# Optimization experiments

Hardware: AMD Instinct MI355X
Metric: run time of the kernel (lower is better)

Reference implementation:

```python
import jax, jax.numpy as jnp
import numpy as np

# Module constants (match init_kwargs / input_specs)
B, Q, K, DM, H, F, S = 2, 2048, 2048, 512, 8, 5, 2
DH = DM // H  # head dim = 64


def setup_inputs() -> dict:
    key = jax.random.key(0)
    ks_ = jax.random.split(key, 18)
    sc = 1.0 / np.sqrt(DM)
    inp = {
        'qs': jax.random.normal(ks_[0], (B, Q, DM), jnp.float32),
        'ks': jax.random.normal(ks_[1], (B, K, DM), jnp.float32),
        'vs': jax.random.normal(ks_[2], (B, K, DM), jnp.float32),
        'qs_locs': jax.random.uniform(ks_[3], (B, Q, S), jnp.float32) * 10.0,
        'ks_locs': jax.random.uniform(ks_[4], (B, K, S), jnp.float32) * 10.0,
        # projection weights (MLP([512]) == single Dense(512))
        'Wq': jax.random.normal(ks_[5], (DM, DM), jnp.float32) * sc,
        'bq': jnp.zeros((DM,), jnp.float32),
        'Wk': jax.random.normal(ks_[6], (DM, DM), jnp.float32) * sc,
        'bk': jnp.zeros((DM,), jnp.float32),
        'Wv': jax.random.normal(ks_[7], (DM, DM), jnp.float32) * sc,
        'bv': jnp.zeros((DM,), jnp.float32),
        'Wo': jax.random.normal(ks_[8], (DM, DM), jnp.float32) * sc,
        'bo': jnp.zeros((DM,), jnp.float32),
        # TISA RBF params, one triple per (head, basis); init near module defaults (1,1,0)
        'a': 1.0 + 0.1 * jax.random.normal(ks_[9], (H * F,), jnp.float32),
        'b': 1.0 + 0.1 * jax.random.normal(ks_[10], (H * F,), jnp.float32),
        'c': 0.1 * jax.random.normal(ks_[11], (H * F,), jnp.float32),
        # valid lens in [K//2, K] so every row has at least one valid key
        'valid_lens': jax.random.randint(ks_[12], (B,), K // 2, K + 1).astype(jnp.int32),
    }
    return inp


def reference(qs, ks, vs, qs_locs, ks_locs, Wq, bq, Wk, bk, Wv, bv, Wo, bo, a, b, c, valid_lens):
    # Projections and head split
    q = (qs @ Wq + bq).reshape(B, Q, H, DH) / jnp.sqrt(jnp.float32(DH))
    k = (ks @ Wk + bk).reshape(B, K, H, DH)
    v = (vs @ Wv + bv).reshape(B, K, H, DH)

    # Pairwise L2 distance between query and key locations: [B, Q, K]
    diff = qs_locs[:, :, None, :] - ks_locs[:, None, :, :]
    d = jnp.sqrt(jnp.sum(diff * diff, axis=-1))

    # TISA RBF bias, summed over F basis functions per head: [B, H, Q, K]
    aH, bH, cH = a.reshape(H, F), b.reshape(H, F), c.reshape(H, F)
    bias = jnp.zeros((B, H, Q, K), jnp.float32)
    for f in range(F):  # small fixed loop over basis functions
        af = aH[:, f][None, :, None, None]
        bf = jnp.abs(bH[:, f])[None, :, None, None]
        cf = cH[:, f][None, :, None, None]
        bias = bias + af * jnp.exp(-bf * (d[:, None] - cf) ** 2)

    scores = jnp.einsum('bqhd,bkhd->bhqk', q, k) + bias
    mask = (jnp.arange(K)[None, :] < valid_lens[:, None])[:, None, None, :]  # [B,1,1,K]
    scores = jnp.where(mask, scores, -jnp.inf)
    p = jax.nn.softmax(scores, axis=-1)  # identical to the online-softmax scan result
    ctx = jnp.einsum('bhqk,bkhd->bqhd', p, v).reshape(B, Q, DM)
    return ctx @ Wo + bo
```

## Files before the change

### kernel.cpp

```cpp
#include <hip/hip_runtime.h>
#include <hip/hip_fp16.h>

typedef unsigned short u16;
typedef __bf16 bf16x8 __attribute__((ext_vector_type(8)));
typedef float f32x4 __attribute__((ext_vector_type(4)));
typedef float f32x16 __attribute__((ext_vector_type(16)));

#define MFMA16(a, b, c) __builtin_amdgcn_mfma_f32_16x16x32_bf16(a, b, c, 0, 0, 0)
#define MFMA32(a, b, c) __builtin_amdgcn_mfma_f32_32x32x16_bf16(a, b, c, 0, 0, 0)

constexpr float LOG2E = 1.44269504088896340736f;

__device__ __forceinline__ u16 f2bf(float x) {
  unsigned u = __float_as_uint(x);
  u += 0x7fffu + ((u >> 16) & 1u);
  return (u16)(u >> 16);
}
__device__ __forceinline__ u16 f2bf_fast(float x) {
  return (u16)((__float_as_uint(x) + 0x8000u) >> 16);
}

struct FalseT { static constexpr bool value = false; };
struct TrueT  { static constexpr bool value = true;  };

__global__ void transpose_w_kernel(const float* __restrict__ w0, const float* __restrict__ w1,
                                   const float* __restrict__ w2, const float* __restrict__ w3,
                                   u16* __restrict__ wt) {
  __shared__ float tile[32][33];
  const float* W = blockIdx.z == 0 ? w0 : blockIdx.z == 1 ? w1 : blockIdx.z == 2 ? w2 : w3;
  u16* T = wt + (size_t)blockIdx.z * 512 * 512;
  int tx = threadIdx.x, ty = threadIdx.y;
  int x = blockIdx.x * 32 + tx;
  int y0 = blockIdx.y * 32;
#pragma unroll
  for (int i = 0; i < 32; i += 8) tile[ty + i][tx] = W[(y0 + ty + i) * 512 + x];
  __syncthreads();
  int xo = blockIdx.y * 32 + tx;
  int r0 = blockIdx.x * 32;
#pragma unroll
  for (int i = 0; i < 32; i += 8) T[(r0 + ty + i) * 512 + xo] = f2bf(tile[tx][ty + i]);
}

__global__ __launch_bounds__(256) void qkv_gemm(
    const float* __restrict__ qs, const float* __restrict__ ks, const float* __restrict__ vs,
    const u16* __restrict__ Wt, const float* __restrict__ bq, const float* __restrict__ bk,
    const float* __restrict__ bv, u16* __restrict__ qg, u16* __restrict__ kg,
    u16* __restrict__ vTg) {
  __shared__ u16 As[128 * 72];
  __shared__ u16 Bs[64 * 72];
  const int tid = threadIdx.x;
  const int wave = tid >> 6, lane = tid & 63;
  const int l15 = lane & 15, quad = lane >> 4;
  const int id = blockIdx.x;
  const bool qk = id < 512;
  int z = 0, m0, n0;
  const float* Af = nullptr;
  const u16* Ab = nullptr;
  const u16* Bb = nullptr;
  const float* Bf = nullptr;
  if (qk) {
    z = id >> 8;
    int t = id & 255;
    m0 = (t >> 3) * 128;
    n0 = (t & 7) * 64;
    Af = z ? ks : qs;
    Bb = Wt + z * 262144;
  } else {
    int t = id - 512;
    m0 = (t >> 6) * 128;
    n0 = (t & 63) * 64;
    Ab = Wt + 2 * 262144;
    Bf = vs;
  }
  f32x4 acc[2][4];
#pragma unroll
  for (int i = 0; i < 2; i++)
#pragma unroll
    for (int j = 0; j < 4; j++) {
      f32x4 zr = {0.f, 0.f, 0.f, 0.f};
      acc[i][j] = zr;
    }
  const int srA = tid >> 1, scA = (tid & 1) * 32;
  const int srB = tid >> 2, scB = (tid & 3) * 16;
  for (int k0 = 0; k0 < 512; k0 += 64) {
    if (qk) {
      const float* ga = Af + (m0 + srA) * 512 + k0 + scA;
      u16* la = As + srA * 72 + scA;
#pragma unroll
      for (int c = 0; c < 4; ++c) {
        float4 f0 = *(const float4*)(ga + c * 8);
        float4 f1 = *(const float4*)(ga + c * 8 + 4);
        uint4 u;
        u.x = f2bf(f0.x) | ((unsigned)f2bf(f0.y) << 16);
        u.y = f2bf(f0.z) | ((unsigned)f2bf(f0.w) << 16);
        u.z = f2bf(f1.x) | ((unsigned)f2bf(f1.y) << 16);
        u.w = f2bf(f1.z) | ((unsigned)f2bf(f1.w) << 16);
        *(uint4*)(la + c * 8) = u;
      }
      const u16* gb = Bb + (n0 + srB) * 512 + k0 + scB;
      u16* lb = Bs + srB * 72 + scB;
      *(uint4*)(lb) = *(const uint4*)(gb);
      *(uint4*)(lb + 8) = *(const uint4*)(gb + 8);
    } else {
      const u16* ga = Ab + (m0 + srA) * 512 + k0 + scA;
      u16* la = As + srA * 72 + scA;
#pragma unroll
      for (int c = 0; c < 4; ++c) *(uint4*)(la + c * 8) = *(const uint4*)(ga + c * 8);
      const float* gb = Bf + (n0 + srB) * 512 + k0 + scB;
      u16* lb = Bs + srB * 72 + scB;
#pragma unroll
      for (int c = 0; c < 2; ++c) {
        float4 f0 = *(const float4*)(gb + c * 8);
        float4 f1 = *(const float4*)(gb + c * 8 + 4);
        uint4 u;
        u.x = f2bf(f0.x) | ((unsigned)f2bf(f0.y) << 16);
        u.y = f2bf(f0.z) | ((unsigned)f2bf(f0.w) << 16);
        u.z = f2bf(f1.x) | ((unsigned)f2bf(f1.y) << 16);
        u.w = f2bf(f1.z) | ((unsigned)f2bf(f1.w) << 16);
        *(uint4*)(lb + c * 8) = u;
      }
    }
    __syncthreads();
#pragma unroll
    for (int st = 0; st < 2; ++st) {
      bf16x8 af[2], bfr[4];
#pragma unroll
      for (int mt = 0; mt < 2; ++mt)
        af[mt] = *(const bf16x8*)(As + (wave * 32 + mt * 16 + l15) * 72 + st * 32 + quad * 8);
#pragma unroll
      for (int nt = 0; nt < 4; ++nt)
        bfr[nt] = *(const bf16x8*)(Bs + (nt * 16 + l15) * 72 + st * 32 + quad * 8);
#pragma unroll
      for (int mt = 0; mt < 2; ++mt)
#pragma unroll
        for (int nt = 0; nt < 4; ++nt) acc[mt][nt] = MFMA16(af[mt], bfr[nt], acc[mt][nt]);
    }
    __syncthreads();
  }
  if (qk) {
    const float* bias = z ? bk : bq;
    const float scale = z ? 1.0f : 0.125f * LOG2E;
#pragma unroll
    for (int mt = 0; mt < 2; ++mt)
#pragma unroll
      for (int nt = 0; nt < 4; ++nt)
#pragma unroll
        for (int r = 0; r < 4; ++r) {
          int row = m0 + wave * 32 + mt * 16 + quad * 4 + r;
          int col = n0 + nt * 16 + l15;
          float v = (acc[mt][nt][r] + bias[col]) * scale;
          int b = row >> 11, key = row & 2047, hh = col >> 6, dh = col & 63;
          int bhh = b * 8 + hh;
          if (z == 0) {
            qg[((bhh * 2048) + key) * 64 + dh] = f2bf(v);
          } else {
            int kt = key >> 6, tt = (key >> 5) & 1, lk = key & 31;
            int st = dh >> 4, hif = (dh >> 3) & 1, j = dh & 7;
            kg[(size_t)(bhh * 32 + kt) * 4096 + tt * 2048 + st * 512 + (hif * 32 + lk) * 8 +
               j] = f2bf(v);
          }
        }
  } else {
#pragma unroll
    for (int mt = 0; mt < 2; ++mt)
#pragma unroll
      for (int nt = 0; nt < 4; ++nt)
#pragma unroll
        for (int r = 0; r < 4; ++r) {
          int row = m0 + wave * 32 + mt * 16 + quad * 4 + r;
          int col = n0 + nt * 16 + l15;
          int hh = row >> 6, dh = row & 63, b = col >> 11, key = col & 2047;
          int bhh = b * 8 + hh;
          int kt = key >> 6, kk = key & 63, st = kk >> 4, hif = (kk >> 3) & 1, j = kk & 7;
          int h2 = dh >> 5, lk = dh & 31;
          vTg[(size_t)(bhh * 32 + kt) * 4096 + h2 * 2048 + st * 512 + (hif * 32 + lk) * 8 + j] =
              f2bf(acc[mt][nt][r] + bv[row]);
        }
  }
}

__global__ __launch_bounds__(256, 4) void attn_kernel(
    const u16* __restrict__ qg, const u16* __restrict__ kfrag, const u16* __restrict__ vfrag,
    const float* __restrict__ qlocs, const float* __restrict__ klocs,
    const float* __restrict__ aP, const float* __restrict__ bP, const float* __restrict__ cP,
    const int* __restrict__ vlen, u16* __restrict__ Opart, float* __restrict__ lpart) {
  constexpr int TBLN = 2048;
  constexpr float DMAX = 14.16f;
  constexpr float TSCALE = (float)TBLN / DMAX;
  __shared__ u16 Ps[4][32 * 68];
  __shared__ alignas(16) float2 klb[576];
  __shared__ float tbl[TBLN];
  const int tid = threadIdx.x;
  const int wave = tid >> 6, lane = tid & 63;
  const int l31 = lane & 31, hi = lane >> 5;
  const int bh = blockIdx.y, b = bh >> 3, h = bh & 7;
  const int z = blockIdx.z;
  const int vl = vlen[b];
  const int ntiles = (vl + 63) >> 6;
  const int nfull = vl >> 6;
  const int tb = ntiles >> 2, rem = ntiles & 3;
  const int kt0 = z * tb + (z < rem ? z : rem);
  const int ktend = kt0 + tb + (z < rem ? 1 : 0);

  for (int i = tid; i < TBLN; i += 256) {
    float d = (i + 0.5f) * (DMAX / TBLN);
    float g = 0.f;
#pragma unroll
    for (int f = 0; f < 5; ++f) {
      float t = d - cP[h * 5 + f];
      g += aP[h * 5 + f] * __expf(-fabsf(bP[h * 5 + f]) * t * t);
    }
    tbl[i] = g * LOG2E;
  }
  const int nk = (ktend - kt0) * 64;
  for (int i = tid; i < nk; i += 256) {
    float2 kl = *(const float2*)(klocs + (b * 2048 + kt0 * 64 + i) * 2);
    klb[i] = make_float2(kl.x * TSCALE, kl.y * TSCALE);
  }
  __syncthreads();

  const int qrow = blockIdx.x * 128 + wave * 32 + l31;
  bf16x8 aq[4];
  {
    const u16* qr = qg + (bh * 2048 + qrow) * 64 + hi * 8;
#pragma unroll
    for (int st = 0; st < 4; ++st) aq[st] = *(const bf16x8*)(qr + st * 16);
  }
  float qpx, qpy;
  {
    float2 p = *(const float2*)(qlocs + (b * 2048 + qrow) * 2);
    qpx = p.x * TSCALE;
    qpy = p.y * TSCALE;
  }
  float l_ = 0.f;
  f32x16 oacc[2];
#pragma unroll
  for (int i = 0; i < 2; ++i)
#pragma unroll
    for (int j = 0; j < 16; ++j) oacc[i][j] = 0.f;
  u16* pw = Ps[wave];

  auto tile = [&](int kt, auto mc) {
    constexpr bool MASKED = decltype(mc)::value;
    const int k0 = kt * 64;
    const int rt64 = (kt - kt0) * 64;
    const u16* fb = kfrag + (size_t)(bh * 32 + kt) * 4096 + lane * 8;
    const u16* vb = vfrag + (size_t)(bh * 32 + kt) * 4096 + lane * 8;
#pragma unroll
    for (int t = 0; t < 2; ++t) {
      bf16x8 kf[4];
#pragma unroll
      for (int st = 0; st < 4; ++st)
        kf[st] = *(const bf16x8*)(fb + t * 2048 + st * 512);
      f32x16 s;
#pragma unroll
      for (int j = 0; j < 16; ++j) s[j] = 0.f;
#pragma unroll
      for (int st = 0; st < 4; ++st) s = MFMA32(kf[st], aq[st], s);
#pragma unroll
      for (int g = 0; g < 4; ++g) {
        const int kl0 = t * 32 + hi * 4 + g * 8;
        float4 ka = *(const float4*)(&klb[rt64 + kl0]);
        float4 kb = *(const float4*)(&klb[rt64 + kl0 + 2]);
        float kx[4] = {ka.x, ka.z, kb.x, kb.z};
        float ky[4] = {ka.y, ka.w, kb.y, kb.w};
        float p[4];
#pragma unroll
        for (int j = 0; j < 4; ++j) {
          float dx = qpx - kx[j], dy = qpy - ky[j];
          float t_ = __builtin_amdgcn_sqrtf(fmaf(dx, dx, dy * dy));
          int ti = (int)t_;
          float v = s[g * 4 + j] + tbl[ti];
          if (MASKED) v = (k0 + kl0 + j < vl) ? v : -1e30f;
          p[j] = __builtin_amdgcn_exp2f(v);
          l_ += p[j];
        }
        uint2 w;
        w.x = f2bf_fast(p[0]) | ((unsigned)f2bf_fast(p[1]) << 16);
        w.y = f2bf_fast(p[2]) | ((unsigned)f2bf_fast(p[3]) << 16);
        *(uint2*)(pw + l31 * 68 + kl0) = w;
      }
    }
    __asm__ volatile("s_waitcnt lgkmcnt(0)" ::: "memory");
    bf16x8 vf[2][4];
#pragma unroll
    for (int h2 = 0; h2 < 2; ++h2)
#pragma unroll
      for (int st = 0; st < 4; ++st)
        vf[h2][st] = *(const bf16x8*)(vb + h2 * 2048 + st * 512);
#pragma unroll
    for (int st = 0; st < 4; ++st) {
      bf16x8 pf = *(const bf16x8*)(pw + l31 * 68 + st * 16 + hi * 8);
#pragma unroll
      for (int h2 = 0; h2 < 2; ++h2) oacc[h2] = MFMA32(vf[h2][st], pf, oacc[h2]);
    }
  };

  const int fullend = ktend < nfull ? ktend : nfull;
  for (int kt = kt0; kt < fullend; ++kt) tile(kt, FalseT{});
  if (ktend > nfull) tile(nfull, TrueT{});

  l_ += __shfl_xor(l_, 32);
  if (hi == 0) lpart[z * 32768 + bh * 2048 + qrow] = l_;
  u16* ob = Opart + ((size_t)(z * 16 + bh) * 2048 + qrow) * 64;
#pragma unroll
  for (int h2 = 0; h2 < 2; ++h2)
#pragma unroll
    for (int g = 0; g < 4; ++g) {
      const int dh0 = h2 * 32 + hi * 4 + g * 8;
      uint2 w;
      w.x = f2bf(oacc[h2][g * 4 + 0]) | ((unsigned)f2bf(oacc[h2][g * 4 + 1]) << 16);
      w.y = f2bf(oacc[h2][g * 4 + 2]) | ((unsigned)f2bf(oacc[h2][g * 4 + 3]) << 16);
      *(uint2*)(ob + dh0) = w;
    }
}

__global__ __launch_bounds__(256) void combine_kernel(const u16* __restrict__ Opart,
                                                      const float* __restrict__ lpart,
                                                      u16* __restrict__ ctxb) {
  const int t = blockIdx.x * 256 + threadIdx.x;
  const int dh8 = (t & 7) * 8;
  const int row = t >> 3;
  float l = 0.f;
#pragma unroll
  for (int zz = 0; zz < 4; ++zz) l += lpart[zz * 32768 + row];
  const float inv = 1.f / l;
  float vals[8];
#pragma unroll
  for (int j = 0; j < 8; ++j) vals[j] = 0.f;
#pragma unroll
  for (int zz = 0; zz < 4; ++zz) {
    bf16x8 o8 = *(const bf16x8*)(Opart + ((size_t)(zz * 32768) + row) * 64 + dh8);
#pragma unroll
    for (int j = 0; j < 8; ++j) vals[j] += (float)o8[j];
  }
  const int bh = row >> 11, q = row & 2047;
  const int b = bh >> 3, h = bh & 7;
  uint4 u;
  u.x = f2bf(vals[0] * inv) | ((unsigned)f2bf(vals[1] * inv) << 16);
  u.y = f2bf(vals[2] * inv) | ((unsigned)f2bf(vals[3] * inv) << 16);
  u.z = f2bf(vals[4] * inv) | ((unsigned)f2bf(vals[5] * inv) << 16);
  u.w = f2bf(vals[6] * inv) | ((unsigned)f2bf(vals[7] * inv) << 16);
  *(uint4*)(ctxb + ((size_t)(b * 2048 + q) * 512 + h * 64 + dh8)) = u;
}

__global__ __launch_bounds__(256) void out_gemm(const u16* __restrict__ ctxb,
                                                const u16* __restrict__ Wt,
                                                const float* __restrict__ bo,
                                                float* __restrict__ out) {
  __shared__ u16 As[64 * 72];
  __shared__ u16 Bs[64 * 72];
  const u16* WoT = Wt + 3 * 262144;
  const int tid = threadIdx.x;
  const int wave = tid >> 6, lane = tid & 63;
  const int l15 = lane & 15, quad = lane >> 4;
  const int m0 = blockIdx.x * 64, n0 = blockIdx.y * 64;
  f32x4 acc[4];
#pragma unroll
  for (int j = 0; j < 4; j++) {
    f32x4 zr = {0.f, 0.f, 0.f, 0.f};
    acc[j] = zr;
  }
  const int sr = tid >> 2, sc = (tid & 3) * 16;
  for (int k0 = 0; k0 < 512; k0 += 64) {
    const u16* ga = ctxb + (m0 + sr) * 512 + k0 + sc;
    u16* la = As + sr * 72 + sc;
    *(uint4*)(la) = *(const uint4*)(ga);
    *(uint4*)(la + 8) = *(const uint4*)(ga + 8);
    const u16* gb = WoT + (n0 + sr) * 512 + k0 + sc;
    u16* lb = Bs + sr * 72 + sc;
    *(uint4*)(lb) = *(const uint4*)(gb);
    *(uint4*)(lb + 8) = *(const uint4*)(gb + 8);
    __syncthreads();
#pragma unroll
    for (int st = 0; st < 2; ++st) {
      bf16x8 af = *(const bf16x8*)(As + (wave * 16 + l15) * 72 + st * 32 + quad * 8);
#pragma unroll
      for (int nt = 0; nt < 4; ++nt) {
        bf16x8 bfr = *(const bf16x8*)(Bs + (nt * 16 + l15) * 72 + st * 32 + quad * 8);
        acc[nt] = MFMA16(af, bfr, acc[nt]);
      }
    }
    __syncthreads();
  }
#pragma unroll
  for (int nt = 0; nt < 4; ++nt)
#pragma unroll
    for (int r = 0; r < 4; ++r) {
      int rrow = m0 + wave * 16 + quad * 4 + r;
      int col = n0 + nt * 16 + l15;
      out[rrow * 512 + col] = acc[nt][r] + bo[col];
    }
}

extern "C" void kernel_launch(void* const* d_in, const int* in_sizes, int n_in, void* d_out,
                              int out_size, void* d_ws, size_t ws_size, hipStream_t stream) {
  const float* qs = (const float*)d_in[0];
  const float* ks = (const float*)d_in[1];
  const float* vs = (const float*)d_in[2];
  const float* qlocs = (const float*)d_in[3];
  const float* klocs = (const float*)d_in[4];
  const float* Wq = (const float*)d_in[5];
  const float* bq = (const float*)d_in[6];
  const float* Wk = (const float*)d_in[7];
  const float* bk = (const float*)d_in[8];
  const float* Wv = (const float*)d_in[9];
  const float* bv = (const float*)d_in[10];
  const float* Wo = (const float*)d_in[11];
  const float* bo = (const float*)d_in[12];
  const float* aP = (const float*)d_in[13];
  const float* bP = (const float*)d_in[14];
  const float* cP = (const float*)d_in[15];
  const int* vlen = (const int*)d_in[16];
  float* out = (float*)d_out;

  u16* Wt = (u16*)d_ws;
  u16* qg = Wt + 4 * 262144;
  u16* kg = qg + 2097152;
  u16* vTg = kg + 2097152;
  u16* Opart = vTg + 2097152;
  float* lpart = (float*)(Opart + (size_t)4 * 2097152);
  u16* ctxb = (u16*)(lpart + 4 * 32768);

  transpose_w_kernel<<<dim3(16, 16, 4), dim3(32, 8), 0, stream>>>(Wq, Wk, Wv, Wo, Wt);
  qkv_gemm<<<768, 256, 0, stream>>>(qs, ks, vs, Wt, bq, bk, bv, qg, kg, vTg);
  attn_kernel<<<dim3(16, 16, 4), 256, 0, stream>>>(qg, kg, vTg, qlocs, klocs, aP, bP, cP, vlen,
                                                   Opart, lpart);
  combine_kernel<<<1024, 256, 0, stream>>>(Opart, lpart, ctxb);
  out_gemm<<<dim3(64, 8), 256, 0, stream>>>(ctxb, Wt, bo, out);
}
```

Measured before the change: 183.0 us.

## Fuse split-K combine into output GEMM and move LDS wait after V loads

Removes the separate combine kernel by having the output projection GEMM sum the four split-K partial outputs and normalize by the summed denominators while staging its A tile. This drops one kernel launch and the ctx write/read round trip. In exchange, each of the 8 column-blocks now redoes the combine and reads the partial buffers eight times. The attention kernel also moves the LDS wait after the V fragment loads so those loads overlap the pending P stores.

```diff
diff --git a/kernel.cpp b/kernel.cpp
--- a/kernel.cpp
+++ b/kernel.cpp
@@ -281,13 +281,13 @@
         *(uint2*)(pw + l31 * 68 + kl0) = w;
       }
     }
-    __asm__ volatile("s_waitcnt lgkmcnt(0)" ::: "memory");
     bf16x8 vf[2][4];
 #pragma unroll
     for (int h2 = 0; h2 < 2; ++h2)
 #pragma unroll
       for (int st = 0; st < 4; ++st)
         vf[h2][st] = *(const bf16x8*)(vb + h2 * 2048 + st * 512);
+    __asm__ volatile("s_waitcnt lgkmcnt(0)" ::: "memory");
 #pragma unroll
     for (int st = 0; st < 4; ++st) {
       bf16x8 pf = *(const bf16x8*)(pw + l31 * 68 + st * 16 + hi * 8);
@@ -315,36 +315,8 @@
     }
 }
 
-__global__ __launch_bounds__(256) void combine_kernel(const u16* __restrict__ Opart,
-                                                      const float* __restrict__ lpart,
-                                                      u16* __restrict__ ctxb) {
-  const int t = blockIdx.x * 256 + threadIdx.x;
-  const int dh8 = (t & 7) * 8;
-  const int row = t >> 3;
-  float l = 0.f;
-#pragma unroll
-  for (int zz = 0; zz < 4; ++zz) l += lpart[zz * 32768 + row];
-  const float inv = 1.f / l;
-  float vals[8];
-#pragma unroll
-  for (int j = 0; j < 8; ++j) vals[j] = 0.f;
-#pragma unroll
-  for (int zz = 0; zz < 4; ++zz) {
-    bf16x8 o8 = *(const bf16x8*)(Opart + ((size_t)(zz * 32768) + row) * 64 + dh8);
-#pragma unroll
-    for (int j = 0; j < 8; ++j) vals[j] += (float)o8[j];
-  }
-  const int bh = row >> 11, q = row & 2047;
-  const int b = bh >> 3, h = bh & 7;
-  uint4 u;
-  u.x = f2bf(vals[0] * inv) | ((unsigned)f2bf(vals[1] * inv) << 16);
-  u.y = f2bf(vals[2] * inv) | ((unsigned)f2bf(vals[3] * inv) << 16);
-  u.z = f2bf(vals[4] * inv) | ((unsigned)f2bf(vals[5] * inv) << 16);
-  u.w = f2bf(vals[6] * inv) | ((unsigned)f2bf(vals[7] * inv) << 16);
-  *(uint4*)(ctxb + ((size_t)(b * 2048 + q) * 512 + h * 64 + dh8)) = u;
-}
-
-__global__ __launch_bounds__(256) void out_gemm(const u16* __restrict__ ctxb,
+__global__ __launch_bounds__(256) void out_gemm(const u16* __restrict__ Opart,
+                                                const float* __restrict__ lpart,
                                                 const u16* __restrict__ Wt,
                                                 const float* __restrict__ bo,
                                                 float* __restrict__ out) {
@@ -362,11 +334,36 @@
     acc[j] = zr;
   }
   const int sr = tid >> 2, sc = (tid & 3) * 16;
+  const int row = m0 + sr, b = row >> 11, qq = row & 2047;
   for (int k0 = 0; k0 < 512; k0 += 64) {
-    const u16* ga = ctxb + (m0 + sr) * 512 + k0 + sc;
+    const int h = k0 >> 6;
+    const int base = (b * 8 + h) * 2048 + qq;
+    float l = lpart[base] + lpart[32768 + base] + lpart[2 * 32768 + base] +
+              lpart[3 * 32768 + base];
+    const float inv = 1.f / l;
+    float vals[16];
+#pragma unroll
+    for (int e = 0; e < 16; ++e) vals[e] = 0.f;
+#pragma unroll
+    for (int zz = 0; zz < 4; ++zz) {
+      const u16* op = Opart + ((size_t)(zz * 32768) + base) * 64 + sc;
+#pragma unroll
+      for (int c = 0; c < 2; ++c) {
+        bf16x8 o8 = *(const bf16x8*)(op + c * 8);
+#pragma unroll
+        for (int j = 0; j < 8; ++j) vals[c * 8 + j] += (float)o8[j];
+      }
+    }
     u16* la = As + sr * 72 + sc;
-    *(uint4*)(la) = *(const uint4*)(ga);
-    *(uint4*)(la + 8) = *(const uint4*)(ga + 8);
+#pragma unroll
+    for (int c = 0; c < 2; ++c) {
+      uint4 u;
+      u.x = f2bf(vals[c * 8 + 0] * inv) | ((unsigned)f2bf(vals[c * 8 + 1] * inv) << 16);
+      u.y = f2bf(vals[c * 8 + 2] * inv) | ((unsigned)f2bf(vals[c * 8 + 3] * inv) << 16);
+      u.z = f2bf(vals[c * 8 + 4] * inv) | ((unsigned)f2bf(vals[c * 8 + 5] * inv) << 16);
+      u.w = f2bf(vals[c * 8 + 6] * inv) | ((unsigned)f2bf(vals[c * 8 + 7] * inv) << 16);
+      *(uint4*)(la + c * 8) = u;
+    }
     const u16* gb = WoT + (n0 + sr) * 512 + k0 + sc;
     u16* lb = Bs + sr * 72 + sc;
     *(uint4*)(lb) = *(const uint4*)(gb);
@@ -420,12 +417,10 @@
   u16* vTg = kg + 2097152;
   u16* Opart = vTg + 2097152;
   float* lpart = (float*)(Opart + (size_t)4 * 2097152);
-  u16* ctxb = (u16*)(lpart + 4 * 32768);
 
   transpose_w_kernel<<<dim3(16, 16, 4), dim3(32, 8), 0, stream>>>(Wq, Wk, Wv, Wo, Wt);
   qkv_gemm<<<768, 256, 0, stream>>>(qs, ks, vs, Wt, bq, bk, bv, qg, kg, vTg);
   attn_kernel<<<dim3(16, 16, 4), 256, 0, stream>>>(qg, kg, vTg, qlocs, klocs, aP, bP, cP, vlen,
                                                    Opart, lpart);
-  combine_kernel<<<1024, 256, 0, stream>>>(Opart, lpart, ctxb);
-  out_gemm<<<dim3(64, 8), 256, 0, stream>>>(ctxb, Wt, bo, out);
-}
+  out_gemm<<<dim3(64, 8), 256, 0, stream>>>(Opart, lpart, Wt, bo, out);
+}
```

Result: no change. 182.8 us, median of 2 (-0.1%).
